# Optimization experiments

Measured on AMD Instinct MI355X. Metric: run time of the kernel, lower is better.

## Reference

```python
import jax, jax.numpy as jnp
import numpy as np

THRESHOLD = 0.05

def binarize101(w, threshold):
    # Ternary quantization to {-1, 0, +1}: zero inside the dead-zone [-thr, thr].
    pos = (w > threshold).astype(w.dtype)
    neg = (w < -threshold).astype(w.dtype)
    return pos - neg

def setup_inputs() -> dict:
    key = jax.random.key(0)
    k1, k2, k3 = jax.random.split(key, 3)
    x = jax.random.normal(k1, (8192, 4096), dtype=jnp.float32)
    weight = jax.random.normal(k2, (4096, 4096), dtype=jnp.float32)
    bias = jax.random.normal(k3, (4096,), dtype=jnp.float32)
    return {"x": x, "weight": weight, "bias": bias}

def reference(x, weight, bias):
    wb = binarize101(weight, THRESHOLD)
    # F.linear: x @ wb.T + bias ; x: [N, in], weight: [out, in] -> [N, out]
    return jnp.einsum('ni,oi->no', x, wb) + bias
```

## Files before the change

### kernel.cpp

```cpp
#include <hip/hip_runtime.h>

typedef float floatx4 __attribute__((ext_vector_type(4)));
typedef __bf16 bf16x8 __attribute__((ext_vector_type(8)));
using u16 = unsigned short;
using u32 = unsigned int;

#define GLOBAL_AS __attribute__((address_space(1)))
#define LDS_AS    __attribute__((address_space(3)))

__global__ void cvt_x_perm(const float* __restrict__ x, u16* __restrict__ xb,
                           int K, int Kd8, int n8) {
  int stride = gridDim.x * blockDim.x;
  for (int i = blockIdx.x * blockDim.x + threadIdx.x; i < n8; i += stride) {
    const int row = i / Kd8;
    const int k = (i - row * Kd8) * 8;
    const float4* p = (const float4*)(x + (size_t)row * K + k);
    float4 a = p[0], b = p[1];
    float v[8] = {a.x, a.y, a.z, a.w, b.x, b.y, b.z, b.w};
    u32 r[8];
#pragma unroll
    for (int j = 0; j < 8; ++j) {
      u32 u = __float_as_uint(v[j]);
      r[j] = (u + 0x7FFFu + ((u >> 16) & 1u)) >> 16;
    }
    uint4 o;
    o.x = r[0] | (r[1] << 16);
    o.y = r[2] | (r[3] << 16);
    o.z = r[4] | (r[5] << 16);
    o.w = r[6] | (r[7] << 16);
    const int pn = row >> 8, rl = row & 255;
    const int g = rl >> 6, rr = rl & 63;
    const int t = k >> 6, kl = k & 63;
    const int tid = ((rr >> 4) << 7) | (((kl >> 5) & 1) << 6) | (((kl >> 3) & 3) << 4) | (rr & 15);
    u16* dst = xb + (size_t)pn * ((size_t)K << 8) + (size_t)t * 16384 + g * 4096 + tid * 8;
    *(uint4*)dst = o;
  }
}

__global__ void quant_w_perm(const float* __restrict__ w, u16* __restrict__ wb,
                             int K, int Kd8, int n8) {
  int stride = gridDim.x * blockDim.x;
  for (int i = blockIdx.x * blockDim.x + threadIdx.x; i < n8; i += stride) {
    const int n = i / Kd8;
    const int k = (i - n * Kd8) * 8;
    const float4* p = (const float4*)(w + (size_t)n * K + k);
    float4 a = p[0], b = p[1];
    float v[8] = {a.x, a.y, a.z, a.w, b.x, b.y, b.z, b.w};
    u32 r[8];
#pragma unroll
    for (int j = 0; j < 8; ++j) {
      r[j] = (v[j] > 0.05f) ? 0x3F80u : ((v[j] < -0.05f) ? 0xBF80u : 0u);
    }
    uint4 o;
    o.x = r[0] | (r[1] << 16);
    o.y = r[2] | (r[3] << 16);
    o.z = r[4] | (r[5] << 16);
    o.w = r[6] | (r[7] << 16);
    const int pn = n >> 8, rl = n & 255;
    const int q = ((rl >> 7) & 1) + (((rl >> 5) & 1) << 1);
    const int t = k >> 6, kl = k & 63;
    const int tid = (((rl >> 6) & 1) << 8) | (((rl >> 4) & 1) << 7) |
                    (((kl >> 5) & 1) << 6) | (((kl >> 3) & 3) << 4) | (rl & 15);
    u16* dst = wb + (size_t)pn * ((size_t)K << 8) + (size_t)t * 16384 + q * 4096 + tid * 8;
    *(uint4*)dst = o;
  }
}

__global__ __launch_bounds__(512, 2) void gemm_bin_lin(
    const u16* __restrict__ Ap, const u16* __restrict__ Bp,
    const float* __restrict__ bias, float* __restrict__ C,
    int M, int N, int K) {
  __shared__ u16 lds[65536];

  const int tid = threadIdx.x;
  const int w = tid >> 6, l = tid & 63;
  const int wr = w >> 2, wc = w & 3;
  const int r = l & 15;

  const int nbn = N >> 8;
  int wg = blockIdx.x;
  const int nwg = gridDim.x;
  if ((nwg & 7) == 0) wg = (wg & 7) * (nwg >> 3) + (wg >> 3);
  const int bm = wg / nbn, bn = wg % nbn;

  const int T = K >> 6;

  const u16* const Abase = Ap + (size_t)bm * ((size_t)K << 8) + tid * 8;
  const u16* const Bbase = Bp + (size_t)bn * ((size_t)K << 8) + tid * 8;

  const u16* const afp0 = lds + wr * 8192 + l * 8;
  const u16* const bfp0 = lds + 16384 + wc * 2048 + l * 8;

  floatx4 acc[8][4] = {};
  bf16x8 af[8], bflo[4], bfhi[4];

#define GLOAD(gptr, u16off)                                                    \
  __builtin_amdgcn_global_load_lds((const GLOBAL_AS void*)(gptr),              \
                                   (LDS_AS void*)(lds + (u16off)), 16, 0, 0)
#define BARRIER __builtin_amdgcn_s_barrier()
#define LGKM0  do { asm volatile("s_waitcnt lgkmcnt(0)" ::: "memory");         \
                    __builtin_amdgcn_sched_barrier(0); } while (0)

  GLOAD(Abase + 0 * 4096,      0 + tid * 8);
  GLOAD(Abase + 2 * 4096,   8192 + tid * 8);
  GLOAD(Bbase + 0 * 4096,  16384 + tid * 8);
  GLOAD(Bbase + 1 * 4096,  20480 + tid * 8);
  GLOAD(Bbase + 2 * 4096,  24576 + tid * 8);
  GLOAD(Bbase + 3 * 4096,  28672 + tid * 8);
  GLOAD(Abase + 1 * 4096,   4096 + tid * 8);
  GLOAD(Abase + 3 * 4096,  12288 + tid * 8);
  asm volatile("s_waitcnt vmcnt(4)" ::: "memory");
  BARRIER;

  for (int t = 0; t < T; ++t) {
    const int bufc = (t & 1) << 15;
    const int bufn = bufc ^ 32768;
    const bool doSt = (t + 1 < T);
    const size_t tn = (size_t)(t + 1) * 16384;

    const u16* afp = afp0 + bufc;
    const u16* bfp = bfp0 + bufc;

#pragma unroll
    for (int i = 0; i < 8; ++i) af[i] = *(const bf16x8*)(afp + i * 512);
#pragma unroll
    for (int i = 0; i < 4; ++i) bflo[i] = *(const bf16x8*)(bfp + i * 512);
    if (doSt) {
      GLOAD(Abase + tn + 0 * 4096, bufn + 0 + tid * 8);
      GLOAD(Abase + tn + 2 * 4096, bufn + 8192 + tid * 8);
    }
    asm volatile("s_waitcnt lgkmcnt(8)" ::: "memory");
    BARRIER;
    LGKM0;
    __builtin_amdgcn_s_setprio(1);
#pragma unroll
    for (int j = 0; j < 2; ++j)
#pragma unroll
      for (int mg = 0; mg < 4; ++mg)
#pragma unroll
        for (int ng = 0; ng < 2; ++ng)
          acc[mg][ng] = __builtin_amdgcn_mfma_f32_16x16x32_bf16(
              af[mg * 2 + j], bflo[ng * 2 + j], acc[mg][ng], 0, 0, 0);
    __builtin_amdgcn_s_setprio(0);
    if (doSt) asm volatile("s_waitcnt vmcnt(4)" ::: "memory");
    else      asm volatile("s_waitcnt vmcnt(2)" ::: "memory");
    BARRIER;

#pragma unroll
    for (int i = 0; i < 4; ++i) bfhi[i] = *(const bf16x8*)(bfp + 8192 + i * 512);
    if (doSt) {
      GLOAD(Bbase + tn + 0 * 4096, bufn + 16384 + tid * 8);
      GLOAD(Bbase + tn + 1 * 4096, bufn + 20480 + tid * 8);
    }
    BARRIER;
    LGKM0;
    __builtin_amdgcn_s_setprio(1);
#pragma unroll
    for (int j = 0; j < 2; ++j)
#pragma unroll
      for (int mg = 0; mg < 4; ++mg)
#pragma unroll
        for (int ng = 0; ng < 2; ++ng)
          acc[mg][2 + ng] = __builtin_amdgcn_mfma_f32_16x16x32_bf16(
              af[mg * 2 + j], bfhi[ng * 2 + j], acc[mg][2 + ng], 0, 0, 0);
    __builtin_amdgcn_s_setprio(0);
    if (doSt) asm volatile("s_waitcnt vmcnt(4)" ::: "memory");
    else      asm volatile("s_waitcnt vmcnt(0)" ::: "memory");
    BARRIER;

#pragma unroll
    for (int i = 0; i < 8; ++i) af[i] = *(const bf16x8*)(afp + 4096 + i * 512);
    if (doSt) {
      GLOAD(Bbase + tn + 2 * 4096, bufn + 24576 + tid * 8);
      GLOAD(Bbase + tn + 3 * 4096, bufn + 28672 + tid * 8);
    }
    asm volatile("s_waitcnt lgkmcnt(4)" ::: "memory");
    BARRIER;
    LGKM0;
    __builtin_amdgcn_s_setprio(1);
#pragma unroll
    for (int j = 0; j < 2; ++j)
#pragma unroll
      for (int mg = 0; mg < 4; ++mg)
#pragma unroll
        for (int ng = 0; ng < 2; ++ng)
          acc[4 + mg][ng] = __builtin_amdgcn_mfma_f32_16x16x32_bf16(
              af[mg * 2 + j], bflo[ng * 2 + j], acc[4 + mg][ng], 0, 0, 0);
    __builtin_amdgcn_s_setprio(0);
    if (doSt) asm volatile("s_waitcnt vmcnt(4)" ::: "memory");
    BARRIER;

    if (doSt) {
      GLOAD(Abase + tn + 1 * 4096, bufn + 4096 + tid * 8);
      GLOAD(Abase + tn + 3 * 4096, bufn + 12288 + tid * 8);
    }
    BARRIER;
    __builtin_amdgcn_s_setprio(1);
#pragma unroll
    for (int j = 0; j < 2; ++j)
#pragma unroll
      for (int mg = 0; mg < 4; ++mg)
#pragma unroll
        for (int ng = 0; ng < 2; ++ng)
          acc[4 + mg][2 + ng] = __builtin_amdgcn_mfma_f32_16x16x32_bf16(
              af[mg * 2 + j], bfhi[ng * 2 + j], acc[4 + mg][2 + ng], 0, 0, 0);
    __builtin_amdgcn_s_setprio(0);
    if (doSt) asm volatile("s_waitcnt vmcnt(4)" ::: "memory");
    BARRIER;
  }
#undef GLOAD
#undef BARRIER
#undef LGKM0

  const int g = l >> 4;
  const int colb = bn * 256 + wc * 64;
  float bv[4];
#pragma unroll
  for (int n = 0; n < 4; ++n) bv[n] = bias[colb + n * 16 + r];
  const int rowb0 = bm * 256 + wr * 128;
#pragma unroll
  for (int m = 0; m < 8; ++m) {
    const int rowb = rowb0 + m * 16 + g * 4;
#pragma unroll
    for (int n = 0; n < 4; ++n) {
      const int col = colb + n * 16 + r;
      float* cp = C + (size_t)rowb * N + col;
#pragma unroll
      for (int q = 0; q < 4; ++q) cp[(size_t)q * N] = acc[m][n][q] + bv[n];
    }
  }
}

__global__ void gemm_naive_kernel(const float* __restrict__ x, const float* __restrict__ wgt,
                                  const float* __restrict__ bias, float* __restrict__ out,
                                  int M, int N, int K) {
  long long idx = (long long)blockIdx.x * blockDim.x + threadIdx.x;
  if (idx >= (long long)M * N) return;
  int o = (int)(idx % N);
  int m = (int)(idx / N);
  const float* xr = x + (size_t)m * K;
  const float* wr = wgt + (size_t)o * K;
  float s = 0.f;
  for (int i = 0; i < K; ++i) {
    float wv = wr[i];
    float t = (wv > 0.05f) ? 1.f : ((wv < -0.05f) ? -1.f : 0.f);
    s = fmaf(xr[i], t, s);
  }
  out[idx] = s + bias[o];
}

extern "C" void kernel_launch(void* const* d_in, const int* in_sizes, int n_in,
                              void* d_out, int out_size, void* d_ws, size_t ws_size,
                              hipStream_t stream) {
  const float* x    = (const float*)d_in[0];
  const float* wgt  = (const float*)d_in[1];
  const float* bias = (const float*)d_in[2];
  float* out = (float*)d_out;

  const int N = in_sizes[2];
  const int K = in_sizes[1] / N;
  const int M = in_sizes[0] / K;

  const size_t need = ((size_t)M * K + (size_t)N * K) * sizeof(u16);
  if (ws_size >= need && (M % 256 == 0) && (N % 256 == 0) && (K % 64 == 0) && K >= 128) {
    u16* xb = (u16*)d_ws;
    u16* wb = xb + (size_t)M * K;
    const int nx8 = (M * K) / 8;
    const int nw8 = (N * K) / 8;
    cvt_x_perm<<<2048, 256, 0, stream>>>(x, xb, K, K / 8, nx8);
    quant_w_perm<<<2048, 256, 0, stream>>>(wgt, wb, K, K / 8, nw8);
    const int grid = (M / 256) * (N / 256);
    gemm_bin_lin<<<grid, 512, 0, stream>>>(xb, wb, bias, out, M, N, K);
  } else {
    const long long total = (long long)M * N;
    gemm_naive_kernel<<<(unsigned)((total + 255) / 256), 256, 0, stream>>>(x, wgt, bias, out, M, N, K);
  }
}
```

Baseline: 357.0 us.

## Switch GEMM to 32x32x16 MFMA and tile the prepass converts through LDS

```diff
diff --git a/kernel.cpp b/kernel.cpp
--- a/kernel.cpp
+++ b/kernel.cpp
@@ -1,6 +1,6 @@
 #include <hip/hip_runtime.h>
 
-typedef float floatx4 __attribute__((ext_vector_type(4)));
+typedef float floatx16 __attribute__((ext_vector_type(16)));
 typedef __bf16 bf16x8 __attribute__((ext_vector_type(8)));
 using u16 = unsigned short;
 using u32 = unsigned int;
@@ -8,65 +8,77 @@
 #define GLOBAL_AS __attribute__((address_space(1)))
 #define LDS_AS    __attribute__((address_space(3)))
 
-__global__ void cvt_x_perm(const float* __restrict__ x, u16* __restrict__ xb,
-                           int K, int Kd8, int n8) {
-  int stride = gridDim.x * blockDim.x;
-  for (int i = blockIdx.x * blockDim.x + threadIdx.x; i < n8; i += stride) {
-    const int row = i / Kd8;
-    const int k = (i - row * Kd8) * 8;
-    const float4* p = (const float4*)(x + (size_t)row * K + k);
-    float4 a = p[0], b = p[1];
-    float v[8] = {a.x, a.y, a.z, a.w, b.x, b.y, b.z, b.w};
-    u32 r[8];
-#pragma unroll
-    for (int j = 0; j < 8; ++j) {
-      u32 u = __float_as_uint(v[j]);
-      r[j] = (u + 0x7FFFu + ((u >> 16) & 1u)) >> 16;
-    }
-    uint4 o;
+__device__ __forceinline__ u32 rne_bf16(float f) {
+  u32 u = __float_as_uint(f);
+  return (u + 0x7FFFu + ((u >> 16) & 1u)) >> 16;
+}
+
+__global__ __launch_bounds__(256) void cvt_x_perm(const float* __restrict__ x,
+                                                  u16* __restrict__ xb, int K) {
+  __shared__ u16 sm[16384];
+  const int tid = threadIdx.x;
+  const int Kt = K >> 6;
+  const int pn = blockIdx.x / Kt, tt = blockIdx.x % Kt;
+  const float* src = x + (size_t)pn * 256 * K + tt * 64;
+#pragma unroll
+  for (int j = 0; j < 16; ++j) {
+    const int fc = j * 256 + tid;
+    const int row = fc >> 4, kl4 = fc & 15;
+    const float4 v = *(const float4*)(src + (size_t)row * K + kl4 * 4);
+    uint2 o;
+    o.x = rne_bf16(v.x) | (rne_bf16(v.y) << 16);
+    o.y = rne_bf16(v.z) | (rne_bf16(v.w) << 16);
+    const int gi = row >> 5, rowin = row & 31;
+    const int ks = kl4 >> 2;
+    const int lane = rowin + 32 * ((kl4 >> 1) & 1);
+    const int e4 = (kl4 & 1) * 4;
+    *(uint2*)(sm + gi * 2048 + ks * 512 + lane * 8 + e4) = o;
+  }
+  __syncthreads();
+  u16* dst = xb + (size_t)pn * 256 * K + (size_t)tt * 16384;
+#pragma unroll
+  for (int j = 0; j < 8; ++j) {
+    const int o = (j * 256 + tid) * 8;
+    *(uint4*)(dst + o) = *(const uint4*)(sm + o);
+  }
+}
+
+__global__ __launch_bounds__(256) void quant_w_perm(const float* __restrict__ w,
+                                                    u16* __restrict__ wb, int K) {
+  __shared__ u16 sm[16384];
+  const int tid = threadIdx.x;
+  const int Kt = K >> 6;
+  const int pn = blockIdx.x / Kt, tt = blockIdx.x % Kt;
+  const float* src = w + (size_t)pn * 256 * K + tt * 64;
+#pragma unroll
+  for (int j = 0; j < 16; ++j) {
+    const int fc = j * 256 + tid;
+    const int row = fc >> 4, kl4 = fc & 15;
+    const float4 v = *(const float4*)(src + (size_t)row * K + kl4 * 4);
+    float vv[4] = {v.x, v.y, v.z, v.w};
+    u32 r[4];
+#pragma unroll
+    for (int e = 0; e < 4; ++e)
+      r[e] = (vv[e] > 0.05f) ? 0x3F80u : ((vv[e] < -0.05f) ? 0xBF80u : 0u);
+    uint2 o;
     o.x = r[0] | (r[1] << 16);
     o.y = r[2] | (r[3] << 16);
-    o.z = r[4] | (r[5] << 16);
-    o.w = r[6] | (r[7] << 16);
-    const int pn = row >> 8, rl = row & 255;
-    const int g = rl >> 6, rr = rl & 63;
-    const int t = k >> 6, kl = k & 63;
-    const int tid = ((rr >> 4) << 7) | (((kl >> 5) & 1) << 6) | (((kl >> 3) & 3) << 4) | (rr & 15);
-    u16* dst = xb + (size_t)pn * ((size_t)K << 8) + (size_t)t * 16384 + g * 4096 + tid * 8;
-    *(uint4*)dst = o;
-  }
-}
-
-__global__ void quant_w_perm(const float* __restrict__ w, u16* __restrict__ wb,
-                             int K, int Kd8, int n8) {
-  int stride = gridDim.x * blockDim.x;
-  for (int i = blockIdx.x * blockDim.x + threadIdx.x; i < n8; i += stride) {
-    const int n = i / Kd8;
-    const int k = (i - n * Kd8) * 8;
-    const float4* p = (const float4*)(w + (size_t)n * K + k);
-    float4 a = p[0], b = p[1];
-    float v[8] = {a.x, a.y, a.z, a.w, b.x, b.y, b.z, b.w};
-    u32 r[8];
-#pragma unroll
-    for (int j = 0; j < 8; ++j) {
-      r[j] = (v[j] > 0.05f) ? 0x3F80u : ((v[j] < -0.05f) ? 0xBF80u : 0u);
-    }
-    uint4 o;
-    o.x = r[0] | (r[1] << 16);
-    o.y = r[2] | (r[3] << 16);
-    o.z = r[4] | (r[5] << 16);
-    o.w = r[6] | (r[7] << 16);
-    const int pn = n >> 8, rl = n & 255;
-    const int q = ((rl >> 7) & 1) + (((rl >> 5) & 1) << 1);
-    const int t = k >> 6, kl = k & 63;
-    const int tid = (((rl >> 6) & 1) << 8) | (((rl >> 4) & 1) << 7) |
-                    (((kl >> 5) & 1) << 6) | (((kl >> 3) & 3) << 4) | (rl & 15);
-    u16* dst = wb + (size_t)pn * ((size_t)K << 8) + (size_t)t * 16384 + q * 4096 + tid * 8;
-    *(uint4*)dst = o;
-  }
-}
-
-__global__ __launch_bounds__(512, 2) void gemm_bin_lin(
+    const int gi = row >> 5, rowin = row & 31;
+    const int ks = kl4 >> 2;
+    const int lane = rowin + 32 * ((kl4 >> 1) & 1);
+    const int e4 = (kl4 & 1) * 4;
+    *(uint2*)(sm + gi * 2048 + ks * 512 + lane * 8 + e4) = o;
+  }
+  __syncthreads();
+  u16* dst = wb + (size_t)pn * 256 * K + (size_t)tt * 16384;
+#pragma unroll
+  for (int j = 0; j < 8; ++j) {
+    const int o = (j * 256 + tid) * 8;
+    *(uint4*)(dst + o) = *(const uint4*)(sm + o);
+  }
+}
+
+__global__ __launch_bounds__(512, 2) void gemm_bin_3232(
     const u16* __restrict__ Ap, const u16* __restrict__ Bp,
     const float* __restrict__ bias, float* __restrict__ C,
     int M, int N, int K) {
@@ -75,7 +87,6 @@
   const int tid = threadIdx.x;
   const int w = tid >> 6, l = tid & 63;
   const int wr = w >> 2, wc = w & 3;
-  const int r = l & 15;
 
   const int nbn = N >> 8;
   int wg = blockIdx.x;
@@ -89,9 +100,9 @@
   const u16* const Bbase = Bp + (size_t)bn * ((size_t)K << 8) + tid * 8;
 
   const u16* const afp0 = lds + wr * 8192 + l * 8;
-  const u16* const bfp0 = lds + 16384 + wc * 2048 + l * 8;
-
-  floatx4 acc[8][4] = {};
+  const u16* const bfp0 = lds + 16384 + wc * 4096 + l * 8;
+
+  floatx16 acc[4][2] = {};
   bf16x8 af[8], bflo[4], bfhi[4];
 
 #define GLOAD(gptr, u16off)                                                    \
@@ -109,7 +120,7 @@
   GLOAD(Bbase + 3 * 4096,  28672 + tid * 8);
   GLOAD(Abase + 1 * 4096,   4096 + tid * 8);
   GLOAD(Abase + 3 * 4096,  12288 + tid * 8);
-  asm volatile("s_waitcnt vmcnt(4)" ::: "memory");
+  asm volatile("s_waitcnt vmcnt(2)" ::: "memory");
   BARRIER;
 
   for (int t = 0; t < T; ++t) {
@@ -122,9 +133,12 @@
     const u16* bfp = bfp0 + bufc;
 
 #pragma unroll
-    for (int i = 0; i < 8; ++i) af[i] = *(const bf16x8*)(afp + i * 512);
-#pragma unroll
-    for (int i = 0; i < 4; ++i) bflo[i] = *(const bf16x8*)(bfp + i * 512);
+    for (int m = 0; m < 2; ++m)
+#pragma unroll
+      for (int ks = 0; ks < 4; ++ks)
+        af[m * 4 + ks] = *(const bf16x8*)(afp + m * 2048 + ks * 512);
+#pragma unroll
+    for (int ks = 0; ks < 4; ++ks) bflo[ks] = *(const bf16x8*)(bfp + ks * 512);
     if (doSt) {
       GLOAD(Abase + tn + 0 * 4096, bufn + 0 + tid * 8);
       GLOAD(Abase + tn + 2 * 4096, bufn + 8192 + tid * 8);
@@ -134,20 +148,18 @@
     LGKM0;
     __builtin_amdgcn_s_setprio(1);
 #pragma unroll
-    for (int j = 0; j < 2; ++j)
-#pragma unroll
-      for (int mg = 0; mg < 4; ++mg)
-#pragma unroll
-        for (int ng = 0; ng < 2; ++ng)
-          acc[mg][ng] = __builtin_amdgcn_mfma_f32_16x16x32_bf16(
-              af[mg * 2 + j], bflo[ng * 2 + j], acc[mg][ng], 0, 0, 0);
+    for (int ks = 0; ks < 4; ++ks)
+#pragma unroll
+      for (int m = 0; m < 2; ++m)
+        acc[m][0] = __builtin_amdgcn_mfma_f32_32x32x16_bf16(
+            af[m * 4 + ks], bflo[ks], acc[m][0], 0, 0, 0);
     __builtin_amdgcn_s_setprio(0);
     if (doSt) asm volatile("s_waitcnt vmcnt(4)" ::: "memory");
     else      asm volatile("s_waitcnt vmcnt(2)" ::: "memory");
     BARRIER;
 
 #pragma unroll
-    for (int i = 0; i < 4; ++i) bfhi[i] = *(const bf16x8*)(bfp + 8192 + i * 512);
+    for (int ks = 0; ks < 4; ++ks) bfhi[ks] = *(const bf16x8*)(bfp + 2048 + ks * 512);
     if (doSt) {
       GLOAD(Bbase + tn + 0 * 4096, bufn + 16384 + tid * 8);
       GLOAD(Bbase + tn + 1 * 4096, bufn + 20480 + tid * 8);
@@ -156,20 +168,21 @@
     LGKM0;
     __builtin_amdgcn_s_setprio(1);
 #pragma unroll
-    for (int j = 0; j < 2; ++j)
-#pragma unroll
-      for (int mg = 0; mg < 4; ++mg)
-#pragma unroll
-        for (int ng = 0; ng < 2; ++ng)
-          acc[mg][2 + ng] = __builtin_amdgcn_mfma_f32_16x16x32_bf16(
-              af[mg * 2 + j], bfhi[ng * 2 + j], acc[mg][2 + ng], 0, 0, 0);
+    for (int ks = 0; ks < 4; ++ks)
+#pragma unroll
+      for (int m = 0; m < 2; ++m)
+        acc[m][1] = __builtin_amdgcn_mfma_f32_32x32x16_bf16(
+            af[m * 4 + ks], bfhi[ks], acc[m][1], 0, 0, 0);
     __builtin_amdgcn_s_setprio(0);
     if (doSt) asm volatile("s_waitcnt vmcnt(4)" ::: "memory");
     else      asm volatile("s_waitcnt vmcnt(0)" ::: "memory");
     BARRIER;
 
 #pragma unroll
-    for (int i = 0; i < 8; ++i) af[i] = *(const bf16x8*)(afp + 4096 + i * 512);
+    for (int m = 0; m < 2; ++m)
+#pragma unroll
+      for (int ks = 0; ks < 4; ++ks)
+        af[m * 4 + ks] = *(const bf16x8*)(afp + 4096 + m * 2048 + ks * 512);
     if (doSt) {
       GLOAD(Bbase + tn + 2 * 4096, bufn + 24576 + tid * 8);
       GLOAD(Bbase + tn + 3 * 4096, bufn + 28672 + tid * 8);
@@ -179,13 +192,11 @@
     LGKM0;
     __builtin_amdgcn_s_setprio(1);
 #pragma unroll
-    for (int j = 0; j < 2; ++j)
-#pragma unroll
-      for (int mg = 0; mg < 4; ++mg)
-#pragma unroll
-        for (int ng = 0; ng < 2; ++ng)
-          acc[4 + mg][ng] = __builtin_amdgcn_mfma_f32_16x16x32_bf16(
-              af[mg * 2 + j], bflo[ng * 2 + j], acc[4 + mg][ng], 0, 0, 0);
+    for (int ks = 0; ks < 4; ++ks)
+#pragma unroll
+      for (int m = 0; m < 2; ++m)
+        acc[2 + m][0] = __builtin_amdgcn_mfma_f32_32x32x16_bf16(
+            af[m * 4 + ks], bflo[ks], acc[2 + m][0], 0, 0, 0);
     __builtin_amdgcn_s_setprio(0);
     if (doSt) asm volatile("s_waitcnt vmcnt(4)" ::: "memory");
     BARRIER;
@@ -197,36 +208,34 @@
     BARRIER;
     __builtin_amdgcn_s_setprio(1);
 #pragma unroll
-    for (int j = 0; j < 2; ++j)
-#pragma unroll
-      for (int mg = 0; mg < 4; ++mg)
-#pragma unroll
-        for (int ng = 0; ng < 2; ++ng)
-          acc[4 + mg][2 + ng] = __builtin_amdgcn_mfma_f32_16x16x32_bf16(
-              af[mg * 2 + j], bfhi[ng * 2 + j], acc[4 + mg][2 + ng], 0, 0, 0);
-    __builtin_amdgcn_s_setprio(0);
-    if (doSt) asm volatile("s_waitcnt vmcnt(4)" ::: "memory");
+    for (int ks = 0; ks < 4; ++ks)
+#pragma unroll
+      for (int m = 0; m < 2; ++m)
+        acc[2 + m][1] = __builtin_amdgcn_mfma_f32_32x32x16_bf16(
+            af[m * 4 + ks], bfhi[ks], acc[2 + m][1], 0, 0, 0);
+    __builtin_amdgcn_s_setprio(0);
+    if (doSt) asm volatile("s_waitcnt vmcnt(2)" ::: "memory");
     BARRIER;
   }
 #undef GLOAD
 #undef BARRIER
 #undef LGKM0
 
-  const int g = l >> 4;
-  const int colb = bn * 256 + wc * 64;
-  float bv[4];
-#pragma unroll
-  for (int n = 0; n < 4; ++n) bv[n] = bias[colb + n * 16 + r];
-  const int rowb0 = bm * 256 + wr * 128;
-#pragma unroll
-  for (int m = 0; m < 8; ++m) {
-    const int rowb = rowb0 + m * 16 + g * 4;
-#pragma unroll
-    for (int n = 0; n < 4; ++n) {
-      const int col = colb + n * 16 + r;
+  const int colq = l & 31;
+  const int hi4 = (l >> 5) * 4;
+#pragma unroll
+  for (int m = 0; m < 4; ++m) {
+    const int rowb = bm * 256 + wr * 128 + m * 32 + hi4;
+#pragma unroll
+    for (int n = 0; n < 2; ++n) {
+      const int col = bn * 256 + wc * 64 + n * 32 + colq;
+      const float bv = bias[col];
       float* cp = C + (size_t)rowb * N + col;
 #pragma unroll
-      for (int q = 0; q < 4; ++q) cp[(size_t)q * N] = acc[m][n][q] + bv[n];
+      for (int q = 0; q < 16; ++q) {
+        const int dr = (q & 3) + 8 * (q >> 2);
+        cp[(size_t)dr * N] = acc[m][n][q] + bv;
+      }
     }
   }
 }
@@ -265,12 +274,11 @@
   if (ws_size >= need && (M % 256 == 0) && (N % 256 == 0) && (K % 64 == 0) && K >= 128) {
     u16* xb = (u16*)d_ws;
     u16* wb = xb + (size_t)M * K;
-    const int nx8 = (M * K) / 8;
-    const int nw8 = (N * K) / 8;
-    cvt_x_perm<<<2048, 256, 0, stream>>>(x, xb, K, K / 8, nx8);
-    quant_w_perm<<<2048, 256, 0, stream>>>(wgt, wb, K, K / 8, nw8);
+    const int Kt = K / 64;
+    cvt_x_perm<<<(M / 256) * Kt, 256, 0, stream>>>(x, xb, K);
+    quant_w_perm<<<(N / 256) * Kt, 256, 0, stream>>>(wgt, wb, K);
     const int grid = (M / 256) * (N / 256);
-    gemm_bin_lin<<<grid, 512, 0, stream>>>(xb, wb, bias, out, M, N, K);
+    gemm_bin_3232<<<grid, 512, 0, stream>>>(xb, wb, bias, out, M, N, K);
   } else {
     const long long total = (long long)M * N;
     gemm_naive_kernel<<<(unsigned)((total + 255) / 256), 256, 0, stream>>>(x, wgt, bias, out, M, N, K);
```

Result: faster. 297.0 us (-16.8%).
